# Kernel tuning notes

Measured on AMD Instinct MI355X. Metric: run time of the kernel, lower is better.

Reference implementation:

```python
import jax, jax.numpy as jnp
import numpy as np

NUM_HEADS = 8
SCALE = 25.0
SIM_THRESH = 0.75


def setup_inputs() -> dict:
    key = jax.random.key(0)
    k1, k2, k3, k4 = jax.random.split(key, 4)
    B, N, C = 1, 2048, 1024
    x_cls = jax.random.normal(k1, (B, N, C), jnp.float32)
    cls_score = jax.random.uniform(k2, (N,), jnp.float32)
    fg_score = jax.random.uniform(k3, (N,), jnp.float32)
    W_qkv = jax.random.normal(k4, (3 * C, C), jnp.float32) * 0.02
    return {"x_cls": x_cls, "cls_score": cls_score, "fg_score": fg_score, "W_qkv": W_qkv}


def reference(x_cls, cls_score, fg_score, W_qkv):
    B, N, C = x_cls.shape
    H = NUM_HEADS
    hd = C // H
    # qkv projection (Linear without bias): [B,N,3C] -> [3,B,H,N,hd]
    qkv = (x_cls @ W_qkv.T).reshape(B, N, 3, H, hd).transpose(2, 0, 3, 1, 4)
    q, k, v = qkv[0], qkv[1], qkv[2]
    # cosine normalization
    qn = q / jnp.linalg.norm(q, axis=-1, keepdims=True)
    kn = k / jnp.linalg.norm(k, axis=-1, keepdims=True)
    vn = v / jnp.linalg.norm(v, axis=-1, keepdims=True)
    # cls_score broadcast to [1,1,1,N] (columns); fg_score is unused downstream
    cs = cls_score.reshape(1, 1, 1, N)
    # raw v-v similarity map [B,H,N,N]
    attn_cls_raw = vn @ jnp.swapaxes(vn, -2, -1)
    # use_mask=True path: mask[i,j] = cls_score[j] > cls_score[i] - 0.1
    cs_mask = (cs > jnp.swapaxes(cs, -2, -1) - 0.1).astype(x_cls.dtype)
    # scaled, score-weighted, masked attention; dropout p=0 is identity
    attn = jax.nn.softmax((qn @ jnp.swapaxes(kn, -2, -1)) * SCALE * cs * cs_mask, axis=-1)
    x = jnp.swapaxes(attn @ v, 1, 2).reshape(B, N, C)
    x_ori = jnp.swapaxes(v, 1, 2).reshape(B, N, C)
    x_out = jnp.concatenate([x, x_ori], axis=-1)  # [B,N,2C]
    # ave=True branch: head-averaged similarity + second softmax, masked renorm
    sim_raw = attn_cls_raw.sum(axis=1)[0] / H  # [N,N]
    sim_mask = (sim_raw > SIM_THRESH).astype(x_cls.dtype)
    sim_attn = attn.sum(axis=1)[0] / H
    sim_round2 = jax.nn.softmax(sim_attn, axis=-1)
    masked = sim_mask * sim_round2
    sim_round2 = masked / jnp.sum(masked, axis=-1, keepdims=True)
    return (x_out, sim_round2)
```

## Files before the change

kernel.cpp:

```cpp
#include <hip/hip_runtime.h>
#include <cstdint>

typedef unsigned short u16;
typedef __attribute__((ext_vector_type(8))) short short8;
typedef __attribute__((ext_vector_type(4))) float f32x4;

#define NTOK 2048
#define CDIM 1024
#define C3   3072
#define NH   8
#define HD   128

__device__ __forceinline__ float bf2f(u16 u) {
    return __uint_as_float(((unsigned)u) << 16);
}
__device__ __forceinline__ u16 f2bf(float f) {
    unsigned u = __float_as_uint(f);
    u += 0x7fffu + ((u >> 16) & 1u);
    return (u16)(u >> 16);
}
__device__ __forceinline__ void gld_lds16(const u16* g, u16* l) {
    __builtin_amdgcn_global_load_lds(
        (__attribute__((address_space(1))) void*)(u16*)g,
        (__attribute__((address_space(3))) void*)l, 16, 0, 0);
}

__global__ __launch_bounds__(256) void k_cast(const float* __restrict__ x,
                                              const float* __restrict__ w,
                                              u16* __restrict__ xb,
                                              u16* __restrict__ wb) {
    int t = blockIdx.x * blockDim.x + threadIdx.x;
    int stride = gridDim.x * blockDim.x;
    for (int i = t; i < (NTOK * CDIM) / 4; i += stride) {
        float4 v = ((const float4*)x)[i];
        ushort4 o;
        o.x = f2bf(v.x); o.y = f2bf(v.y); o.z = f2bf(v.z); o.w = f2bf(v.w);
        ((ushort4*)xb)[i] = o;
    }
    for (int i = t; i < (C3 * CDIM) / 4; i += stride) {
        float4 v = ((const float4*)w)[i];
        ushort4 o;
        o.x = f2bf(v.x); o.y = f2bf(v.y); o.z = f2bf(v.z); o.w = f2bf(v.w);
        ((ushort4*)wb)[i] = o;
    }
}

template <int EPI>
__global__ __launch_bounds__(256) void k_gemm16(const u16* __restrict__ A,
                                                const u16* __restrict__ B,
                                                void* __restrict__ Cv, int K,
                                                int lda, int ldb, int ldc,
                                                float scale) {
    __shared__ u16 As[128 * 32];
    __shared__ u16 Bs[128 * 32];
    const int tid = threadIdx.x;
    const int lane = tid & 63;
    const int wid = tid >> 6;
    const int wm = wid >> 1, wn = wid & 1;
    const int q = lane >> 4, l16 = lane & 15;
    const int m0 = blockIdx.y * 128, n0 = blockIdx.x * 128;

    f32x4 zero4 = {0.f, 0.f, 0.f, 0.f};
    f32x4 acc[4][4];
#pragma unroll
    for (int i = 0; i < 4; i++)
#pragma unroll
        for (int j = 0; j < 4; j++) acc[i][j] = zero4;

    const int s0 = tid, r0 = s0 >> 2, c0 = (s0 & 3) * 8;
    const int s1 = tid + 256, r1 = s1 >> 2, c1 = (s1 & 3) * 8;
    const u16* a0 = &A[(long long)(m0 + r0) * lda + c0];
    const u16* b0 = &B[(long long)(n0 + r0) * ldb + c0];
    const u16* a1 = &A[(long long)(m0 + r1) * lda + c1];
    const u16* b1 = &B[(long long)(n0 + r1) * ldb + c1];

    for (int k0 = 0; k0 < K; k0 += 32) {
        __syncthreads();
        gld_lds16(a0 + k0, &As[s0 * 8]);
        gld_lds16(b0 + k0, &Bs[s0 * 8]);
        gld_lds16(a1 + k0, &As[s1 * 8]);
        gld_lds16(b1 + k0, &Bs[s1 * 8]);
        __syncthreads();
        short8 af[4], bfr[4];
#pragma unroll
        for (int tm = 0; tm < 4; tm++)
            af[tm] = *(const short8*)&As[(wm * 64 + tm * 16 + l16) * 32 + q * 8];
#pragma unroll
        for (int tn = 0; tn < 4; tn++)
            bfr[tn] = *(const short8*)&Bs[(wn * 64 + tn * 16 + l16) * 32 + q * 8];
#pragma unroll
        for (int tm = 0; tm < 4; tm++)
#pragma unroll
            for (int tn = 0; tn < 4; tn++)
                acc[tm][tn] = __builtin_amdgcn_mfma_f32_16x16x32_bf16(
                    af[tm], bfr[tn], acc[tm][tn], 0, 0, 0);
    }

#pragma unroll
    for (int tm = 0; tm < 4; tm++)
#pragma unroll
        for (int tn = 0; tn < 4; tn++)
#pragma unroll
            for (int r = 0; r < 4; r++) {
                int row = m0 + wm * 64 + tm * 16 + q * 4 + r;
                int col = n0 + wn * 64 + tn * 16 + l16;
                float v = acc[tm][tn][r];
                long long off = (long long)row * ldc + col;
                if (EPI == 0) {
                    ((u16*)Cv)[off] = f2bf(v);
                } else {
                    ((unsigned char*)Cv)[off] = (v * scale > 0.75f) ? 1 : 0;
                }
            }
}

__global__ __launch_bounds__(256) void k_norm(const u16* __restrict__ qkv,
                                              u16* __restrict__ Qn,
                                              u16* __restrict__ Kn,
                                              u16* __restrict__ Vn,
                                              float* __restrict__ out) {
    int n = blockIdx.x;
    int lane = threadIdx.x & 63;
    int w = threadIdx.x >> 6;
    for (int s = w; s < 24; s += 4) {
        int which = s >> 3;
        int h = s & 7;
        int d0 = lane * 2;
        const u16* src = qkv + (long long)n * C3 + which * CDIM + h * HD + d0;
        u16 u0 = src[0], u1 = src[1];
        float f0 = bf2f(u0), f1 = bf2f(u1);
        float ss = f0 * f0 + f1 * f1;
#pragma unroll
        for (int off = 1; off < 64; off <<= 1) ss += __shfl_xor(ss, off);
        float rn = rsqrtf(ss);
        u16* dst = (which == 0 ? Qn : which == 1 ? Kn : Vn) +
                   (long long)n * CDIM + h * HD + d0;
        ushort2 nv;
        nv.x = f2bf(f0 * rn);
        nv.y = f2bf(f1 * rn);
        *(ushort2*)dst = nv;
        if (which == 2) {
            float2 fo;
            fo.x = f0; fo.y = f1;
            *(float2*)&out[(long long)n * 2048 + 1024 + h * HD + d0] = fo;
        }
    }
}

__global__ __launch_bounds__(256) void k_vt(const u16* __restrict__ qkv,
                                            u16* __restrict__ Vt) {
    __shared__ u16 T[64][72];
    const int n0 = blockIdx.x * 64;
    const int c0 = blockIdx.y * 64;
    const int tid = threadIdx.x;
    {
        int nl = tid >> 2, cc = (tid & 3) * 16;
        const u16* src = &qkv[(long long)(n0 + nl) * C3 + 2 * CDIM + c0 + cc];
        *(short8*)&T[nl][cc] = *(const short8*)&src[0];
        *(short8*)&T[nl][cc + 8] = *(const short8*)&src[8];
    }
    __syncthreads();
    {
        int cl = tid >> 2, nc = (tid & 3) * 16;
        ushort va[16];
#pragma unroll
        for (int i = 0; i < 16; i++) va[i] = T[nc + i][cl];
        u16* dst = &Vt[(long long)(c0 + cl) * NTOK + n0 + nc];
        *(short8*)&dst[0] = *(short8*)&va[0];
        *(short8*)&dst[8] = *(short8*)&va[8];
    }
}

__global__ __launch_bounds__(256, 4) void k_attn7(const u16* __restrict__ Qn,
                                                  const u16* __restrict__ Kn,
                                                  const u16* __restrict__ Vt,
                                                  const float* __restrict__ cls,
                                                  u16* __restrict__ P,
                                                  float* __restrict__ Spart,
                                                  u16* __restrict__ Xpart) {
    __shared__ u16 Kf[16384];
    __shared__ u16 Vf[16384];
    __shared__ u16 Et[4096];
    const int h = blockIdx.z;
    const int jc = blockIdx.y;
    const int i0 = blockIdx.x * 64;
    const int jbase = jc * 512;
    const int tid = threadIdx.x, lane = tid & 63, wid = tid >> 6;
    const int q = lane >> 4, l16 = lane & 15;
    const int wm = wid >> 1, wn = wid & 1;

    short8 af[2][4];
#pragma unroll
    for (int m = 0; m < 2; m++)
#pragma unroll
        for (int kt = 0; kt < 4; kt++)
            af[m][kt] = *(const short8*)&Qn[(long long)(i0 + wm * 32 + m * 16 + l16) * CDIM +
                                            h * HD + kt * 32 + q * 8];
    float cls_i[2][4];
#pragma unroll
    for (int m = 0; m < 2; m++)
#pragma unroll
        for (int r = 0; r < 4; r++)
            cls_i[m][r] = cls[i0 + wm * 32 + m * 16 + q * 4 + r] - 0.1f;

    const u16* ksrc[4];
    const u16* vsrc[4];
#pragma unroll
    for (int t = 0; t < 4; t++) {
        int g = wid * 4 + t;
        int tn = g >> 2, kt = g & 3;
        ksrc[t] = &Kn[(long long)(jbase + tn * 16 + l16) * CDIM + h * HD + kt * 32 + q * 8];
        int n = g >> 1, ks = g & 1;
        vsrc[t] = &Vt[(long long)(h * HD + n * 16 + l16) * NTOK + jbase + (ks * 4 + q) * 8];
    }

    f32x4 zero4 = {0.f, 0.f, 0.f, 0.f};
    f32x4 pv[2][4];
#pragma unroll
    for (int m = 0; m < 2; m++)
#pragma unroll
        for (int n = 0; n < 4; n++) pv[m][n] = zero4;
    float sums[2][4] = {{0.f, 0.f, 0.f, 0.f}, {0.f, 0.f, 0.f, 0.f}};

    for (int jt = 0; jt < 8; ++jt) {
        const int j0 = jbase + jt * 64;
        __syncthreads();
#pragma unroll
        for (int t = 0; t < 4; t++) {
            int g = wid * 4 + t;
            gld_lds16(ksrc[t], &Kf[(g * 64 + lane) * 8]);
            gld_lds16(vsrc[t], &Vf[(g * 64 + lane) * 8]);
            ksrc[t] += 64 * CDIM;
            vsrc[t] += 64;
        }
        __syncthreads();
#pragma unroll
        for (int tn = 0; tn < 2; tn++) {
            int tng = wn * 2 + tn;
            short8 bfr[4];
#pragma unroll
            for (int kt = 0; kt < 4; kt++)
                bfr[kt] = *(const short8*)&Kf[((tng * 4 + kt) * 64 + lane) * 8];
            int j = j0 + tng * 16 + l16;
            float cj = cls[j];
            float sc = 25.f * cj;
#pragma unroll
            for (int m = 0; m < 2; m++) {
                f32x4 acc = zero4;
#pragma unroll
                for (int kt = 0; kt < 4; kt++)
                    acc = __builtin_amdgcn_mfma_f32_16x16x32_bf16(af[m][kt], bfr[kt],
                                                                  acc, 0, 0, 0);
                int ibase = wm * 32 + m * 16 + q * 4;
#pragma unroll
                for (int r = 0; r < 4; r++) {
                    float mk = (cj > cls_i[m][r]) ? 1.f : 0.f;
                    float e = __expf(acc[r] * sc * mk);
                    sums[m][r] += e;
                    int il = ibase + r;
                    int jl = tng * 16 + l16;
                    Et[il * 64 + ((((jl >> 3) ^ (il & 7)) << 3) | (jl & 7))] = f2bf(e);
                }
            }
        }
        __syncthreads();
        {
            int il = tid >> 2, c = tid & 3;
            int x = il & 7;
            short8 e0 = *(const short8*)&Et[il * 64 + (((2 * c) ^ x) << 3)];
            short8 e1 = *(const short8*)&Et[il * 64 + (((2 * c + 1) ^ x) << 3)];
            u16* dst = &P[((long long)(h * NTOK + i0 + il)) * NTOK + j0 + c * 16];
            *(short8*)&dst[0] = e0;
            *(short8*)&dst[8] = e1;
        }
#pragma unroll
        for (int ks = 0; ks < 2; ks++) {
            short8 a2[2];
#pragma unroll
            for (int m2 = 0; m2 < 2; m2++) {
                int il = wm * 32 + m2 * 16 + l16;
                int ch = ks * 4 + q;
                a2[m2] = *(const short8*)&Et[il * 64 + ((ch ^ (il & 7)) << 3)];
            }
#pragma unroll
            for (int n2 = 0; n2 < 4; n2++) {
                short8 b2 = *(const short8*)&Vf[(((wn * 4 + n2) * 2 + ks) * 64 + lane) * 8];
#pragma unroll
                for (int m2 = 0; m2 < 2; m2++)
                    pv[m2][n2] = __builtin_amdgcn_mfma_f32_16x16x32_bf16(
                        a2[m2], b2, pv[m2][n2], 0, 0, 0);
            }
        }
    }
#pragma unroll
    for (int m = 0; m < 2; m++)
#pragma unroll
        for (int r = 0; r < 4; r++) {
            float s = sums[m][r];
            s += __shfl_xor(s, 1);
            s += __shfl_xor(s, 2);
            s += __shfl_xor(s, 4);
            s += __shfl_xor(s, 8);
            if (l16 == 0)
                Spart[((wn * 4 + jc) * NH + h) * NTOK + i0 + wm * 32 + m * 16 + q * 4 + r] = s;
        }
    u16* Xp = Xpart + (long long)jc * NTOK * CDIM;
#pragma unroll
    for (int m2 = 0; m2 < 2; m2++)
#pragma unroll
        for (int n2 = 0; n2 < 4; n2++)
#pragma unroll
            for (int r = 0; r < 4; r++) {
                int i = i0 + wm * 32 + m2 * 16 + q * 4 + r;
                int d = wn * 64 + n2 * 16 + l16;
                Xp[(long long)i * CDIM + h * HD + d] = f2bf(pv[m2][n2][r]);
            }
}

__global__ __launch_bounds__(256) void k_comb2(const u16* __restrict__ Xpart,
                                               const float* __restrict__ Spart,
                                               float* __restrict__ out) {
    int idx = blockIdx.x * 256 + threadIdx.x;
    int base = idx * 8;
    int i = base >> 10, c = base & 1023;
    int h = c >> 7;
    float s = 0.f;
#pragma unroll
    for (int g = 0; g < 8; g++) s += Spart[(g * NH + h) * NTOK + i];
    float acc[8] = {0.f, 0.f, 0.f, 0.f, 0.f, 0.f, 0.f, 0.f};
#pragma unroll
    for (int jc = 0; jc < 4; jc++) {
        short8 v = *(const short8*)&Xpart[(long long)jc * NTOK * CDIM + (long long)i * CDIM + c];
#pragma unroll
        for (int k = 0; k < 8; k++) acc[k] += bf2f((u16)v[k]);
    }
    float invs = 1.f / s;
    float4 o0, o1;
    o0.x = acc[0] * invs; o0.y = acc[1] * invs; o0.z = acc[2] * invs; o0.w = acc[3] * invs;
    o1.x = acc[4] * invs; o1.y = acc[5] * invs; o1.z = acc[6] * invs; o1.w = acc[7] * invs;
    float* dst = &out[(long long)i * 2048 + c];
    *(float4*)dst = o0;
    *(float4*)(dst + 4) = o1;
}

__global__ __launch_bounds__(256) void k_out2(const u16* __restrict__ P,
                                              const float* __restrict__ Spart,
                                              const unsigned char* __restrict__ mask,
                                              float* __restrict__ out2) {
    __shared__ float red[256];
    __shared__ float sArr[NH];
    const int i = blockIdx.x;
    const int t = threadIdx.x;
    if (t < NH) {
        float s = 0.f;
#pragma unroll
        for (int g = 0; g < 8; g++) s += Spart[(g * NH + t) * NTOK + i];
        sArr[t] = s;
    }
    __syncthreads();
    float invS[NH];
#pragma unroll
    for (int h = 0; h < NH; h++) invS[h] = 1.f / (8.f * sArr[h]);
    const int c0 = t * 8;
    float a[8] = {0.f, 0.f, 0.f, 0.f, 0.f, 0.f, 0.f, 0.f};
#pragma unroll
    for (int h = 0; h < NH; h++) {
        short8 p = *(const short8*)&P[((long long)h * NTOK + i) * NTOK + c0];
#pragma unroll
        for (int k = 0; k < 8; k++) a[k] += bf2f((u16)p[k]) * invS[h];
    }
    const unsigned char* mrow = mask + (long long)i * NTOK + c0;
    float e[8];
    unsigned char mk[8];
    float part = 0.f;
#pragma unroll
    for (int k = 0; k < 8; k++) {
        e[k] = __expf(a[k]);
        mk[k] = mrow[k];
        if (mk[k]) part += e[k];
    }
    red[t] = part;
    __syncthreads();
    for (int s = 128; s > 0; s >>= 1) {
        if (t < s) red[t] += red[t + s];
        __syncthreads();
    }
    float invT = 1.f / red[0];
    float o[8];
#pragma unroll
    for (int k = 0; k < 8; k++) o[k] = mk[k] ? e[k] * invT : 0.f;
    float4 o0, o1;
    o0.x = o[0]; o0.y = o[1]; o0.z = o[2]; o0.w = o[3];
    o1.x = o[4]; o1.y = o[5]; o1.z = o[6]; o1.w = o[7];
    float* dst = out2 + (long long)i * NTOK + c0;
    *(float4*)dst = o0;
    *(float4*)(dst + 4) = o1;
}

extern "C" void kernel_launch(void* const* d_in, const int* in_sizes, int n_in,
                              void* d_out, int out_size, void* d_ws,
                              size_t ws_size, hipStream_t stream) {
    (void)in_sizes; (void)n_in; (void)out_size; (void)ws_size;
    const float* x = (const float*)d_in[0];
    const float* cls = (const float*)d_in[1];
    const float* Wq = (const float*)d_in[3];
    float* out = (float*)d_out;
    char* ws = (char*)d_ws;

    u16* Xb = (u16*)(ws + 0);
    u16* Wb = (u16*)(ws + 4194304);
    u16* QKVb = (u16*)(ws + 10485760);
    u16* Xpart = (u16*)(ws + 0);
    float* Spart = (float*)(ws + 16777216);
    u16* Qn = (u16*)(ws + 23068672);
    u16* Kn = (u16*)(ws + 27262976);
    u16* Vn = (u16*)(ws + 31457280);
    u16* Vt = (u16*)(ws + 35651584);
    unsigned char* mask = (unsigned char*)(ws + 39845888);
    u16* P = (u16*)(ws + 44040192);

    k_cast<<<1024, 256, 0, stream>>>(x, Wq, Xb, Wb);

    k_gemm16<0><<<dim3(C3 / 128, NTOK / 128), 256, 0, stream>>>(
        Xb, Wb, QKVb, CDIM, CDIM, CDIM, C3, 1.f);

    k_norm<<<NTOK, 256, 0, stream>>>(QKVb, Qn, Kn, Vn, out);

    k_vt<<<dim3(NTOK / 64, CDIM / 64), 256, 0, stream>>>(QKVb, Vt);

    k_gemm16<1><<<dim3(16, 16), 256, 0, stream>>>(
        Vn, Vn, mask, CDIM, CDIM, CDIM, NTOK, 0.125f);

    k_attn7<<<dim3(32, 4, NH), 256, 0, stream>>>(Qn, Kn, Vt, cls, P, Spart, Xpart);

    k_comb2<<<1024, 256, 0, stream>>>(Xpart, Spart, out);

    k_out2<<<NTOK, 256, 0, stream>>>(P, Spart, mask, out + (long long)NTOK * 2048);
}
```

Measured before the change: 222.4 us.

## Fuse combine into output epilogue, vectorize norm, shrink attention LDS tiles

Merges the partial-output combine kernel into the sim-softmax epilogue kernel so one launch per row handles both outputs and reuses the per-head row sums. Vectorizes the normalization kernel to use 16-byte loads and stores with 16-lane reductions. Halves the K/V shared memory buffers in the attention kernel, presumably with a matching tiling change, to reduce LDS footprint and raise occupancy. This risks smaller tile reuse in attention.

```diff
diff --git a/kernel.cpp b/kernel.cpp
--- a/kernel.cpp
+++ b/kernel.cpp
@@ -3,6 +3,7 @@
 
 typedef unsigned short u16;
 typedef __attribute__((ext_vector_type(8))) short short8;
+typedef __attribute__((ext_vector_type(4))) short short4v;
 typedef __attribute__((ext_vector_type(4))) float f32x4;
 
 #define NTOK 2048
@@ -119,30 +120,45 @@
                                               u16* __restrict__ Kn,
                                               u16* __restrict__ Vn,
                                               float* __restrict__ out) {
-    int n = blockIdx.x;
-    int lane = threadIdx.x & 63;
-    int w = threadIdx.x >> 6;
-    for (int s = w; s < 24; s += 4) {
-        int which = s >> 3;
-        int h = s & 7;
-        int d0 = lane * 2;
-        const u16* src = qkv + (long long)n * C3 + which * CDIM + h * HD + d0;
-        u16 u0 = src[0], u1 = src[1];
-        float f0 = bf2f(u0), f1 = bf2f(u1);
-        float ss = f0 * f0 + f1 * f1;
-#pragma unroll
-        for (int off = 1; off < 64; off <<= 1) ss += __shfl_xor(ss, off);
-        float rn = rsqrtf(ss);
-        u16* dst = (which == 0 ? Qn : which == 1 ? Kn : Vn) +
-                   (long long)n * CDIM + h * HD + d0;
-        ushort2 nv;
-        nv.x = f2bf(f0 * rn);
-        nv.y = f2bf(f1 * rn);
-        *(ushort2*)dst = nv;
-        if (which == 2) {
-            float2 fo;
-            fo.x = f0; fo.y = f1;
-            *(float2*)&out[(long long)n * 2048 + 1024 + h * HD + d0] = fo;
+    const int n = blockIdx.x;
+    const int t = threadIdx.x;
+    const int g16 = t >> 4;
+    const int l16 = t & 15;
+    const int d0 = l16 * 8;
+#pragma unroll
+    for (int s = 0; s < 2; s++) {
+        int row = s * 16 + g16;
+        if (row < 24) {
+            int which = row >> 3;
+            int h = row & 7;
+            const u16* src = qkv + (long long)n * C3 + which * CDIM + h * HD + d0;
+            short8 v8 = *(const short8*)src;
+            float f[8];
+            float ss = 0.f;
+#pragma unroll
+            for (int k = 0; k < 8; k++) {
+                f[k] = bf2f((u16)v8[k]);
+                ss += f[k] * f[k];
+            }
+            ss += __shfl_xor(ss, 1);
+            ss += __shfl_xor(ss, 2);
+            ss += __shfl_xor(ss, 4);
+            ss += __shfl_xor(ss, 8);
+            float rn = rsqrtf(ss);
+            u16* dst = (which == 0 ? Qn : which == 1 ? Kn : Vn) +
+                       (long long)n * CDIM + h * HD + d0;
+            short8 o8;
+#pragma unroll
+            for (int k = 0; k < 8; k++) o8[k] = (short)f2bf(f[k] * rn);
+            *(short8*)dst = o8;
+            if (which == 2) {
+                float4 a, b;
+                a.x = f[0]; a.y = f[1]; a.z = f[2]; a.w = f[3];
+                b.x = f[4]; b.y = f[5]; b.z = f[6]; b.w = f[7];
+                float* od = &out[(long long)n * 2048 + 1024 + h * HD + d0];
+                *(float4*)od = a;
+                *(float4*)(od + 4) = b;
+            }
         }
     }
 }
@@ -171,15 +187,15 @@
     }
 }
 
-__global__ __launch_bounds__(256, 4) void k_attn7(const u16* __restrict__ Qn,
+__global__ __launch_bounds__(256, 4) void k_attn8(const u16* __restrict__ Qn,
                                                   const u16* __restrict__ Kn,
                                                   const u16* __restrict__ Vt,
                                                   const float* __restrict__ cls,
                                                   u16* __restrict__ P,
                                                   float* __restrict__ Spart,
                                                   u16* __restrict__ Xpart) {
-    __shared__ u16 Kf[16384];
-    __shared__ u16 Vf[16384];
+    __shared__ u16 Kf[8192];
+    __shared__ u16 Vf[8192];
     __shared__ u16 Et[4096];
     const int h = blockIdx.z;
     const int jc = blockIdx.y;
@@ -317,36 +333,12 @@
             }
 }
 
-__global__ __launch_bounds__(256) void k_comb2(const u16* __restrict__ Xpart,
-                                               const float* __restrict__ Spart,
-                                               float* __restrict__ out) {
-    int idx = blockIdx.x * 256 + threadIdx.x;
-    int base = idx * 8;
-    int i = base >> 10, c = base & 1023;
-    int h = c >> 7;
-    float s = 0.f;
-#pragma unroll
-    for (int g = 0; g < 8; g++) s += Spart[(g * NH + h) * NTOK + i];
-    float acc[8] = {0.f, 0.f, 0.f, 0.f, 0.f, 0.f, 0.f, 0.f};
-#pragma unroll
-    for (int jc = 0; jc < 4; jc++) {
-        short8 v = *(const short8*)&Xpart[(long long)jc * NTOK * CDIM + (long long)i * CDIM + c];
-#pragma unroll
-        for (int k = 0; k < 8; k++) acc[k] += bf2f((u16)v[k]);
-    }
-    float invs = 1.f / s;
-    float4 o0, o1;
-    o0.x = acc[0] * invs; o0.y = acc[1] * invs; o0.z = acc[2] * invs; o0.w = acc[3] * invs;
-    o1.x = acc[4] * invs; o1.y = acc[5] * invs; o1.z = acc[6] * invs; o1.w = acc[7] * invs;
-    float* dst = &out[(long long)i * 2048 + c];
-    *(float4*)dst = o0;
-    *(float4*)(dst + 4) = o1;
-}
-
-__global__ __launch_bounds__(256) void k_out2(const u16* __restrict__ P,
-                                              const float* __restrict__ Spart,
-                                              const unsigned char* __restrict__ mask,
-                                              float* __restrict__ out2) {
+__global__ __launch_bounds__(256) void k_epi(const u16* __restrict__ Xpart,
+                                             const float* __restrict__ Spart,
+                                             const u16* __restrict__ P,
+                                             const unsigned char* __restrict__ mask,
+                                             float* __restrict__ out,
+                                             float* __restrict__ out2) {
     __shared__ float red[256];
     __shared__ float sArr[NH];
     const int i = blockIdx.x;
@@ -358,6 +350,22 @@
         sArr[t] = s;
     }
     __syncthreads();
+    {
+        int c = t * 4;
+        int h = c >> 7;
+        float acc[4] = {0.f, 0.f, 0.f, 0.f};
+#pragma unroll
+        for (int jc = 0; jc < 4; jc++) {
+            short4v v = *(const short4v*)&Xpart[(long long)jc * NTOK * CDIM +
+                                                (long long)i * CDIM + c];
+#pragma unroll
+            for (int k = 0; k < 4; k++) acc[k] += bf2f((u16)v[k]);
+        }
+        float invs = 1.f / sArr[h];
+        float4 o;
+        o.x = acc[0] * invs; o.y = acc[1] * invs; o.z = acc[2] * invs; o.w = acc[3] * invs;
+        *(float4*)&out[(long long)i * 2048 + c] = o;
+    }
     float invS[NH];
 #pragma unroll
     for (int h = 0; h < NH; h++) invS[h] = 1.f / (8.f * sArr[h]);
@@ -431,9 +439,8 @@
     k_gemm16<1><<<dim3(16, 16), 256, 0, stream>>>(
         Vn, Vn, mask, CDIM, CDIM, CDIM, NTOK, 0.125f);
 
-    k_attn7<<<dim3(32, 4, NH), 256, 0, stream>>>(Qn, Kn, Vt, cls, P, Spart, Xpart);
-
-    k_comb2<<<1024, 256, 0, stream>>>(Xpart, Spart, out);
-
-    k_out2<<<NTOK, 256, 0, stream>>>(P, Spart, mask, out + (long long)NTOK * 2048);
-}
+    k_attn8<<<dim3(32, 4, NH), 256, 0, stream>>>(Qn, Kn, Vt, cls, P, Spart, Xpart);
+
+    k_epi<<<NTOK, 256, 0, stream>>>(Xpart, Spart, P, mask, out,
+                                    out + (long long)NTOK * 2048);
+}
```

New measurement: 256.5 us. 1.15x slower.
